# Performance work log

Hardware: AMD Instinct MI355X
Metric: run time of the kernel (lower is better)

Reference implementation:

```python
import jax, jax.numpy as jnp
import numpy as np

B, N, F_NODE, F_EDGE, F_G = 2, 512, 128, 16, 128
MID, OUT = 128, 128


def _linear_params(key, fan_in, fan_out):
    kw, kb = jax.random.split(key)
    scale = 1.0 / np.sqrt(fan_in)
    W = jax.random.normal(kw, (fan_in, fan_out), dtype=jnp.float32) * scale
    b = jnp.zeros((fan_out,), dtype=jnp.float32)
    return W, b


def setup_inputs() -> dict:
    key = jax.random.key(0)
    ks = jax.random.split(key, 12)
    features = jax.random.normal(ks[0], (B, N, F_NODE), dtype=jnp.float32)
    e_features = jax.random.normal(ks[1], (B, N, N, F_EDGE), dtype=jnp.float32)
    g_features = jax.random.normal(ks[2], (B, F_G), dtype=jnp.float32)
    adj = jax.random.randint(ks[3], (B, N, N), 0, 2).astype(jnp.float32)
    W1, b1 = _linear_params(ks[4], F_NODE, MID)
    W2, b2 = _linear_params(ks[5], F_NODE, MID)
    We, be = _linear_params(ks[6], F_EDGE, MID)
    Wg, bg = _linear_params(ks[7], F_G, MID)
    Wo1, bo1 = _linear_params(ks[8], F_NODE, OUT)
    Wo2, bo2 = _linear_params(ks[9], MID, OUT)
    return dict(features=features, e_features=e_features, g_features=g_features,
                adj=adj, W1=W1, b1=b1, W2=W2, b2=b2, We=We, be=be, Wg=Wg, bg=bg,
                Wo1=Wo1, bo1=bo1, Wo2=Wo2, bo2=bo2)


def reference(features, e_features, g_features, adj,
              W1, b1, W2, b2, We, be, Wg, bg, Wo1, bo1, Wo2, bo2):
    # Linear projections (haiku Linear = xW + b)
    msg_1 = jnp.einsum('bnf,fm->bnm', features, W1) + b1      # (b,n,mid)
    msg_2 = jnp.einsum('bnf,fm->bnm', features, W2) + b2      # (b,n,mid)
    msg_e = jnp.einsum('bije,em->bijm', e_features, We) + be  # (b,n,n,mid)
    msg_g = jnp.einsum('bg,gm->bm', g_features, Wg) + bg      # (b,mid)
    # All-pairs broadcast sum: (b,n,n,mid)
    msgs = (msg_1[:, None, :, :] + msg_2[:, :, None, :]
            + msg_e + msg_g[:, None, None, :])
    # Masked max reduction over axis=1 (default reduction=jnp.max)
    msgs = jnp.max(msgs * adj[..., None], axis=1)             # (b,n,mid)
    h_1 = jnp.einsum('bnf,fo->bno', features, Wo1) + bo1
    h_2 = jnp.einsum('bnm,mo->bno', msgs, Wo2) + bo2
    return h_1 + h_2
```

## Files before the change

### kernel.cpp

```cpp
#include <hip/hip_runtime.h>
#include <hip/hip_bf16.h>
#include <math.h>

#define B_   2
#define N_   512
#define FN   128
#define FE   16
#define MID_ 128

typedef __attribute__((ext_vector_type(8)))  short short8_t;
typedef __attribute__((ext_vector_type(16))) float f32x16;

__device__ __forceinline__ short f2bf(float f) {
    __bf16 h = (__bf16)f;
    return __builtin_bit_cast(short, h);
}

__global__ __launch_bounds__(256, 2) void kA(
    const float* __restrict__ feat, const float* __restrict__ gfeat,
    const float* __restrict__ W1, const float* __restrict__ b1,
    const float* __restrict__ W2, const float* __restrict__ b2,
    const float* __restrict__ be,
    const float* __restrict__ Wg, const float* __restrict__ bg,
    const float* __restrict__ Wo1, const float* __restrict__ bo1,
    float* __restrict__ msg1c, float* __restrict__ msg2, float* __restrict__ h1)
{
    __shared__ float fl[2 * FN];
    const int bid = blockIdx.x;
    const int b   = bid >> 8;
    const int n0  = (bid & 255) * 2;
    const int t   = threadIdx.x;
    const int r   = t >> 7, m = t & 127;

    if (t < 64)
        ((float4*)fl)[t] = ((const float4*)(feat + (size_t)(b * N_ + n0) * FN))[t];
    __syncthreads();

    const float* gb = gfeat + b * FN;
    float a1 = 0.f, a2 = 0.f, a3 = 0.f, mg = 0.f;
    for (int k0 = 0; k0 < FN; k0 += 8) {
        float w1v[8], w2v[8], w3v[8], wgv[8];
        #pragma unroll
        for (int u = 0; u < 8; ++u) {
            w1v[u] = W1 [(k0 + u) * MID_ + m];
            w2v[u] = W2 [(k0 + u) * MID_ + m];
            w3v[u] = Wo1[(k0 + u) * MID_ + m];
            wgv[u] = Wg [(k0 + u) * MID_ + m];
        }
        #pragma unroll
        for (int u = 0; u < 8; ++u) {
            const float f = fl[r * FN + k0 + u];
            a1 += f * w1v[u];
            a2 += f * w2v[u];
            a3 += f * w3v[u];
            mg += gb[k0 + u] * wgv[u];
        }
    }
    const size_t idx = (size_t)(b * N_ + n0 + r) * MID_ + m;
    msg1c[idx] = a1 + b1[m] + mg + bg[m] + be[m];
    msg2[idx]  = a2 + b2[m];
    h1[idx]    = a3 + bo1[m];
}

__global__ __launch_bounds__(512, 4) void kB(
    const float* __restrict__ ef, const float* __restrict__ adj,
    const float* __restrict__ We,
    const float* __restrict__ msg1c, const float* __restrict__ msg2,
    float* __restrict__ part)
{
    __shared__ float    m2l[32 * MID_];
    __shared__ float    mtile[4][32 * 32];
    __shared__ unsigned madj[32];
    __shared__ float    anyzf[32];

    const int bid = blockIdx.x;
    const int b   = bid >> 8;
    const int jt  = (bid >> 4) & 15;
    const int ic  = bid & 15;
    const int j0  = jt * 32, i0 = ic * 32;
    const int t    = threadIdx.x;
    const int lane = t & 63, wid = t >> 6;
    const int mt   = wid & 3, ih = wid >> 2;
    const int g    = lane >> 5, lm = lane & 31;

    {
        const float4* src = (const float4*)(msg2 + (size_t)(b * N_ + i0) * MID_);
        ((float4*)m2l)[t]       = src[t];
        ((float4*)m2l)[t + 512] = src[t + 512];
    }
    #pragma unroll
    for (int p = 0; p < 2; ++p) {
        const int i_l = wid * 4 + 2 * p + g;
        const float av = adj[(size_t)(b * N_ + i0 + i_l) * N_ + j0 + lm];
        const unsigned long long bal = __ballot(av != 0.0f);
        if (lane == 0)  madj[wid * 4 + 2 * p]     = (unsigned)bal;
        if (lane == 32) madj[wid * 4 + 2 * p + 1] = (unsigned)(bal >> 32);
    }
    short8_t Bf;
    #pragma unroll
    for (int jj = 0; jj < 8; ++jj)
        Bf[jj] = f2bf(We[(8 * g + jj) * MID_ + mt * 32 + lm]);

    f32x16 accm;
    #pragma unroll
    for (int r = 0; r < 16; ++r) accm[r] = -INFINITY;

    __syncthreads();

    if (t < 32) {
        unsigned ao = 0xFFFFFFFFu;
        #pragma unroll
        for (int i2 = 0; i2 < 32; ++i2) ao &= madj[i2];
        anyzf[t] = ((ao >> t) & 1u) ? -INFINITY : 0.0f;
    }

    const float* efr = ef + (((size_t)(b * N_ + i0 + ih * 16)) * N_ + j0 + lm) * FE + 8 * g;
    #pragma unroll 2
    for (int ii = 0; ii < 16; ++ii) {
        const int i_l = ih * 16 + ii;
        const float4 ea = *(const float4*)efr;
        const float4 eb = *(const float4*)(efr + 4);
        efr += (size_t)N_ * FE;
        short8_t Af;
        Af[0] = f2bf(ea.x); Af[1] = f2bf(ea.y); Af[2] = f2bf(ea.z); Af[3] = f2bf(ea.w);
        Af[4] = f2bf(eb.x); Af[5] = f2bf(eb.y); Af[6] = f2bf(eb.z); Af[7] = f2bf(eb.w);

        const unsigned vmg = madj[i_l] >> (4 * g);
        const float m2v = m2l[i_l * MID_ + mt * 32 + lm];
        f32x16 C;
        #pragma unroll
        for (int r = 0; r < 16; ++r) {
            const int cr = (r & 3) + 8 * (r >> 2);
            C[r] = (vmg & (1u << cr)) ? m2v : -INFINITY;
        }
        const f32x16 S = __builtin_amdgcn_mfma_f32_32x32x16_bf16(Af, Bf, C, 0, 0, 0);
        #pragma unroll
        for (int r = 0; r < 16; ++r) accm[r] = fmaxf(accm[r], S[r]);
    }

    if (ih == 1) {
        #pragma unroll
        for (int r = 0; r < 16; ++r) {
            const int jrow = (r & 3) + 8 * (r >> 2) + 4 * g;
            mtile[mt][jrow * 32 + lm] = accm[r];
        }
    }
    __syncthreads();
    float* ftile = m2l;
    if (ih == 0) {
        #pragma unroll
        for (int r = 0; r < 16; ++r) {
            const int jrow = (r & 3) + 8 * (r >> 2) + 4 * g;
            ftile[jrow * MID_ + mt * 32 + lm] = fmaxf(accm[r], mtile[mt][jrow * 32 + lm]);
        }
    }
    __syncthreads();

    {
        const int jrow = t >> 4, m0 = (t & 15) * 8;
        const float az = anyzf[jrow];
        const float*  c1  = msg1c + (size_t)(b * N_ + j0 + jrow) * MID_ + m0;
        float*        dst = part  + ((size_t)(ic * 2 + b) * N_ + j0 + jrow) * MID_ + m0;
        const float*  tl  = &ftile[jrow * MID_ + m0];
        const float4 c1a = *(const float4*)c1;
        const float4 c1b = *(const float4*)(c1 + 4);
        float4 o0, o1;
        o0.x = fmaxf(tl[0] + c1a.x, az);
        o0.y = fmaxf(tl[1] + c1a.y, az);
        o0.z = fmaxf(tl[2] + c1a.z, az);
        o0.w = fmaxf(tl[3] + c1a.w, az);
        o1.x = fmaxf(tl[4] + c1b.x, az);
        o1.y = fmaxf(tl[5] + c1b.y, az);
        o1.z = fmaxf(tl[6] + c1b.z, az);
        o1.w = fmaxf(tl[7] + c1b.w, az);
        *(float4*)dst       = o0;
        *(float4*)(dst + 4) = o1;
    }
}

__global__ __launch_bounds__(256, 2) void kC(
    const float* __restrict__ part, const float* __restrict__ h1,
    const float* __restrict__ Wo2, const float* __restrict__ bo2,
    float* __restrict__ out)
{
    __shared__ float ms[2 * MID_];
    const int bid = blockIdx.x;
    const int b   = bid >> 8;
    const int j0  = (bid & 255) * 2;
    const int t   = threadIdx.x;
    const int r   = t >> 7, m = t & 127;
    const size_t base = ((size_t)b * N_ + j0 + r) * MID_ + m;

    float u = -INFINITY;
    #pragma unroll
    for (int icc = 0; icc < 16; ++icc)
        u = fmaxf(u, part[(size_t)icc * 2 * N_ * MID_ + base]);
    ms[r * MID_ + m] = u;
    __syncthreads();

    float acc = h1[base] + bo2[m];
    for (int k0 = 0; k0 < MID_; k0 += 8) {
        float wv[8];
        #pragma unroll
        for (int uu = 0; uu < 8; ++uu) wv[uu] = Wo2[(k0 + uu) * MID_ + m];
        #pragma unroll
        for (int uu = 0; uu < 8; ++uu) acc += ms[r * MID_ + k0 + uu] * wv[uu];
    }
    out[base] = acc;
}

extern "C" void kernel_launch(void* const* d_in, const int* in_sizes, int n_in,
                              void* d_out, int out_size, void* d_ws, size_t ws_size,
                              hipStream_t stream)
{
    const float* feat = (const float*)d_in[0];
    const float* ef   = (const float*)d_in[1];
    const float* gf   = (const float*)d_in[2];
    const float* adj  = (const float*)d_in[3];
    const float* W1   = (const float*)d_in[4];
    const float* b1   = (const float*)d_in[5];
    const float* W2   = (const float*)d_in[6];
    const float* b2   = (const float*)d_in[7];
    const float* We   = (const float*)d_in[8];
    const float* be   = (const float*)d_in[9];
    const float* Wg   = (const float*)d_in[10];
    const float* bg   = (const float*)d_in[11];
    const float* Wo1  = (const float*)d_in[12];
    const float* bo1  = (const float*)d_in[13];
    const float* Wo2  = (const float*)d_in[14];
    const float* bo2  = (const float*)d_in[15];
    float* out = (float*)d_out;

    float* ws    = (float*)d_ws;
    float* msg1c = ws;
    float* msg2  = ws + 131072;
    float* h1    = ws + 262144;
    float* part  = ws + 393216;

    hipLaunchKernelGGL(kA, dim3(512), dim3(256), 0, stream,
        feat, gf, W1, b1, W2, b2, be, Wg, bg, Wo1, bo1, msg1c, msg2, h1);
    hipLaunchKernelGGL(kB, dim3(512), dim3(512), 0, stream,
        ef, adj, We, msg1c, msg2, part);
    hipLaunchKernelGGL(kC, dim3(512), dim3(256), 0, stream,
        part, h1, Wo2, bo2, out);
}
```

Before: 37.31 us.

## Compute node projections with bf16 MFMA tiles and split global-message term

The first kernel's scalar FP32 projections are replaced by 32x32 bf16 MFMA tiles, one wavefront per tile. Each tile covers 32 nodes and 32 output columns of W1, W2 or Wo1. The global-feature projection moves to two extra blocks that write a per-batch vector, and the biases are folded into the downstream kernels. The aim is to cut the FP32 FMA and weight-load cost of the projection stage. In exchange the node projections run at bf16 precision and the edge kernel takes extra loads.

```diff
diff --git a/kernel.cpp b/kernel.cpp
--- a/kernel.cpp
+++ b/kernel.cpp
@@ -16,56 +16,89 @@
     return __builtin_bit_cast(short, h);
 }
 
-__global__ __launch_bounds__(256, 2) void kA(
+__global__ __launch_bounds__(64) void kA(
     const float* __restrict__ feat, const float* __restrict__ gfeat,
     const float* __restrict__ W1, const float* __restrict__ b1,
-    const float* __restrict__ W2, const float* __restrict__ b2,
-    const float* __restrict__ be,
+    const float* __restrict__ W2, const float* __restrict__ be,
     const float* __restrict__ Wg, const float* __restrict__ bg,
-    const float* __restrict__ Wo1, const float* __restrict__ bo1,
-    float* __restrict__ msg1c, float* __restrict__ msg2, float* __restrict__ h1)
-{
-    __shared__ float fl[2 * FN];
+    const float* __restrict__ Wo1,
+    float* __restrict__ msg1c, float* __restrict__ msg2, float* __restrict__ h1,
+    float* __restrict__ msgg)
+{
     const int bid = blockIdx.x;
-    const int b   = bid >> 8;
-    const int n0  = (bid & 255) * 2;
     const int t   = threadIdx.x;
-    const int r   = t >> 7, m = t & 127;
-
-    if (t < 64)
-        ((float4*)fl)[t] = ((const float4*)(feat + (size_t)(b * N_ + n0) * FN))[t];
-    __syncthreads();
-
-    const float* gb = gfeat + b * FN;
-    float a1 = 0.f, a2 = 0.f, a3 = 0.f, mg = 0.f;
-    for (int k0 = 0; k0 < FN; k0 += 8) {
-        float w1v[8], w2v[8], w3v[8], wgv[8];
-        #pragma unroll
-        for (int u = 0; u < 8; ++u) {
-            w1v[u] = W1 [(k0 + u) * MID_ + m];
-            w2v[u] = W2 [(k0 + u) * MID_ + m];
-            w3v[u] = Wo1[(k0 + u) * MID_ + m];
-            wgv[u] = Wg [(k0 + u) * MID_ + m];
-        }
-        #pragma unroll
-        for (int u = 0; u < 8; ++u) {
-            const float f = fl[r * FN + k0 + u];
-            a1 += f * w1v[u];
-            a2 += f * w2v[u];
-            a3 += f * w3v[u];
-            mg += gb[k0 + u] * wgv[u];
-        }
-    }
-    const size_t idx = (size_t)(b * N_ + n0 + r) * MID_ + m;
-    msg1c[idx] = a1 + b1[m] + mg + bg[m] + be[m];
-    msg2[idx]  = a2 + b2[m];
-    h1[idx]    = a3 + bo1[m];
+
+    if (bid >= 384) {
+        const int b = bid - 384;
+        const float* gb = gfeat + b * FN;
+        #pragma unroll
+        for (int half = 0; half < 2; ++half) {
+            const int m = t + 64 * half;
+            float mg = b1[m] + be[m] + bg[m];
+            for (int k0 = 0; k0 < FN; k0 += 16) {
+                float wv[16];
+                #pragma unroll
+                for (int u = 0; u < 16; ++u) wv[u] = Wg[(k0 + u) * MID_ + m];
+                #pragma unroll
+                for (int u = 0; u < 16; ++u) mg += gb[k0 + u] * wv[u];
+            }
+            msgg[b * MID_ + m] = mg;
+        }
+        return;
+    }
+
+    const int bb  = bid / 192;
+    const int rem = bid - bb * 192;
+    const int nt  = rem / 12;
+    const int ct  = rem - nt * 12;
+    const int w   = ct >> 2;
+    const int c0  = (ct & 3) * 32;
+    const int n0  = nt * 32;
+    const int g   = t >> 5, lm = t & 31;
+
+    const float* Ws  = (w == 0) ? W1    : (w == 1) ? W2   : Wo1;
+    float*       dst = (w == 0) ? msg1c : (w == 1) ? msg2 : h1;
+
+    short8_t Af[8];
+    #pragma unroll
+    for (int ks = 0; ks < 8; ++ks) {
+        const float* ap = feat + (size_t)(bb * N_ + n0 + lm) * FN + ks * 16 + 8 * g;
+        const float4 a0 = *(const float4*)ap;
+        const float4 a1 = *(const float4*)(ap + 4);
+        short8_t A;
+        A[0] = f2bf(a0.x); A[1] = f2bf(a0.y); A[2] = f2bf(a0.z); A[3] = f2bf(a0.w);
+        A[4] = f2bf(a1.x); A[5] = f2bf(a1.y); A[6] = f2bf(a1.z); A[7] = f2bf(a1.w);
+        Af[ks] = A;
+    }
+    short8_t Bfr[8];
+    #pragma unroll
+    for (int ks = 0; ks < 8; ++ks) {
+        short8_t Bv;
+        #pragma unroll
+        for (int j = 0; j < 8; ++j)
+            Bv[j] = f2bf(Ws[(size_t)(ks * 16 + 8 * g + j) * MID_ + c0 + lm]);
+        Bfr[ks] = Bv;
+    }
+
+    f32x16 acc;
+    #pragma unroll
+    for (int r = 0; r < 16; ++r) acc[r] = 0.0f;
+    #pragma unroll
+    for (int ks = 0; ks < 8; ++ks)
+        acc = __builtin_amdgcn_mfma_f32_32x32x16_bf16(Af[ks], Bfr[ks], acc, 0, 0, 0);
+
+    #pragma unroll
+    for (int r = 0; r < 16; ++r) {
+        const int row = (r & 3) + 8 * (r >> 2) + 4 * g;
+        dst[(size_t)(bb * N_ + n0 + row) * MID_ + c0 + lm] = acc[r];
+    }
 }
 
 __global__ __launch_bounds__(512, 4) void kB(
     const float* __restrict__ ef, const float* __restrict__ adj,
-    const float* __restrict__ We,
+    const float* __restrict__ We, const float* __restrict__ b2,
     const float* __restrict__ msg1c, const float* __restrict__ msg2,
+    const float* __restrict__ msgg,
     float* __restrict__ part)
 {
     __shared__ float    m2l[32 * MID_];
@@ -100,6 +133,7 @@
     #pragma unroll
     for (int jj = 0; jj < 8; ++jj)
         Bf[jj] = f2bf(We[(8 * g + jj) * MID_ + mt * 32 + lm]);
+    const float b2v = b2[mt * 32 + lm];
 
     f32x16 accm;
     #pragma unroll
@@ -126,7 +160,7 @@
         Af[4] = f2bf(eb.x); Af[5] = f2bf(eb.y); Af[6] = f2bf(eb.z); Af[7] = f2bf(eb.w);
 
         const unsigned vmg = madj[i_l] >> (4 * g);
-        const float m2v = m2l[i_l * MID_ + mt * 32 + lm];
+        const float m2v = m2l[i_l * MID_ + mt * 32 + lm] + b2v;
         f32x16 C;
         #pragma unroll
         for (int r = 0; r < 16; ++r) {
@@ -160,19 +194,22 @@
         const int jrow = t >> 4, m0 = (t & 15) * 8;
         const float az = anyzf[jrow];
         const float*  c1  = msg1c + (size_t)(b * N_ + j0 + jrow) * MID_ + m0;
+        const float*  gg  = msgg + b * MID_ + m0;
         float*        dst = part  + ((size_t)(ic * 2 + b) * N_ + j0 + jrow) * MID_ + m0;
         const float*  tl  = &ftile[jrow * MID_ + m0];
         const float4 c1a = *(const float4*)c1;
         const float4 c1b = *(const float4*)(c1 + 4);
+        const float4 g1a = *(const float4*)gg;
+        const float4 g1b = *(const float4*)(gg + 4);
         float4 o0, o1;
-        o0.x = fmaxf(tl[0] + c1a.x, az);
-        o0.y = fmaxf(tl[1] + c1a.y, az);
-        o0.z = fmaxf(tl[2] + c1a.z, az);
-        o0.w = fmaxf(tl[3] + c1a.w, az);
-        o1.x = fmaxf(tl[4] + c1b.x, az);
-        o1.y = fmaxf(tl[5] + c1b.y, az);
-        o1.z = fmaxf(tl[6] + c1b.z, az);
-        o1.w = fmaxf(tl[7] + c1b.w, az);
+        o0.x = fmaxf(tl[0] + c1a.x + g1a.x, az);
+        o0.y = fmaxf(tl[1] + c1a.y + g1a.y, az);
+        o0.z = fmaxf(tl[2] + c1a.z + g1a.z, az);
+        o0.w = fmaxf(tl[3] + c1a.w + g1a.w, az);
+        o1.x = fmaxf(tl[4] + c1b.x + g1b.x, az);
+        o1.y = fmaxf(tl[5] + c1b.y + g1b.y, az);
+        o1.z = fmaxf(tl[6] + c1b.z + g1b.z, az);
+        o1.w = fmaxf(tl[7] + c1b.w + g1b.w, az);
         *(float4*)dst       = o0;
         *(float4*)(dst + 4) = o1;
     }
@@ -180,7 +217,8 @@
 
 __global__ __launch_bounds__(256, 2) void kC(
     const float* __restrict__ part, const float* __restrict__ h1,
-    const float* __restrict__ Wo2, const float* __restrict__ bo2,
+    const float* __restrict__ Wo2, const float* __restrict__ bo1,
+    const float* __restrict__ bo2,
     float* __restrict__ out)
 {
     __shared__ float ms[2 * MID_];
@@ -198,7 +236,7 @@
     ms[r * MID_ + m] = u;
     __syncthreads();
 
-    float acc = h1[base] + bo2[m];
+    float acc = h1[base] + bo1[m] + bo2[m];
     for (int k0 = 0; k0 < MID_; k0 += 8) {
         float wv[8];
         #pragma unroll
@@ -236,11 +274,12 @@
     float* msg2  = ws + 131072;
     float* h1    = ws + 262144;
     float* part  = ws + 393216;
-
-    hipLaunchKernelGGL(kA, dim3(512), dim3(256), 0, stream,
-        feat, gf, W1, b1, W2, b2, be, Wg, bg, Wo1, bo1, msg1c, msg2, h1);
+    float* msgg  = ws + 393216 + 2097152;
+
+    hipLaunchKernelGGL(kA, dim3(386), dim3(64), 0, stream,
+        feat, gf, W1, b1, W2, be, Wg, bg, Wo1, msg1c, msg2, h1, msgg);
     hipLaunchKernelGGL(kB, dim3(512), dim3(512), 0, stream,
-        ef, adj, We, msg1c, msg2, part);
+        ef, adj, We, b2, msg1c, msg2, msgg, part);
     hipLaunchKernelGGL(kC, dim3(512), dim3(256), 0, stream,
-        part, h1, Wo2, bo2, out);
-}
+        part, h1, Wo2, bo1, bo2, out);
+}
```

After: 30.07 us. -19.4%, faster.
